# Kernel tuning notes

Measured on AMD Instinct MI355X. Metric: run time of the kernel, lower is better.

The kernel has to match this reference:

```python
import jax, jax.numpy as jnp
import numpy as np

N, E, IN_DIM, H, D = 40000, 640000, 128, 8, 16


def setup_inputs() -> dict:
    key = jax.random.key(0)
    k_h, k_s, k_d, k_q, k_k, k_v = jax.random.split(key, 6)
    scale = float(np.sqrt(2.0 / (IN_DIM + H * D)))  # xavier-ish
    return {
        "h": jax.random.normal(k_h, (N, IN_DIM), dtype=jnp.float32),
        "src": jax.random.randint(k_s, (E,), 0, N, dtype=jnp.int32),
        "dst": jax.random.randint(k_d, (E,), 0, N, dtype=jnp.int32),
        "WQ": jax.random.normal(k_q, (IN_DIM, H * D), dtype=jnp.float32) * scale,
        "WK": jax.random.normal(k_k, (IN_DIM, H * D), dtype=jnp.float32) * scale,
        "WV": jax.random.normal(k_v, (IN_DIM, H * D), dtype=jnp.float32) * scale,
    }


def reference(h, src, dst, WQ, WK, WV):
    n = h.shape[0]
    Q = (h @ WQ).reshape(n, H, D)  # [N,H,D]
    K = (h @ WK).reshape(n, H, D)
    V = (h @ WV).reshape(n, H, D)
    inv_sqrt_d = 1.0 / jnp.sqrt(jnp.asarray(D, dtype=h.dtype))
    # per-edge elementwise score (DGL u_mul_v keeps the H x D vector)
    score = K[src] * Q[dst] * inv_sqrt_d  # [E,H,D]
    wV = jax.ops.segment_sum(V[src] * score, dst, num_segments=n)  # [N,H,D]
    z = jax.ops.segment_sum(score, dst, num_segments=n)            # [N,H,D]
    return wV / (z + 1e-6)
```

## Files before the change

### kernel.cpp

```cpp
#include <hip/hip_runtime.h>


#define FMA4(acc, s, b) do { \
    (acc).x = fmaf((s), (b).x, (acc).x); \
    (acc).y = fmaf((s), (b).y, (acc).y); \
    (acc).z = fmaf((s), (b).z, (acc).z); \
    (acc).w = fmaf((s), (b).w, (acc).w); } while (0)

__global__ __launch_bounds__(256) void gemm_qkv(
    const float* __restrict__ h,
    const float* __restrict__ WQ,
    const float* __restrict__ WK,
    const float* __restrict__ WV,
    float* __restrict__ Qf,
    float* __restrict__ Kf,
    float* __restrict__ Vf,
    int N)
{
    __shared__ float4 Wl[128 * 32];
    __shared__ float4 Hl[32 * 32];
    const int t = threadIdx.x;
    const int which = blockIdx.y;
    const float* Wsel = (which == 0) ? WQ : ((which == 1) ? WK : WV);
    float* Osel = (which == 0) ? Qf : ((which == 1) ? Kf : Vf);
    const float4* W4 = (const float4*)Wsel;
#pragma unroll
    for (int i = 0; i < 16; ++i) Wl[t + i * 256] = W4[t + i * 256];

    const int c4 = t & 31;
    const int r4 = t >> 5;

    for (int sub = 0; sub < 4; ++sub) {
        const int r0 = (blockIdx.x * 4 + sub) * 32;
        if (r0 >= N) break;
        __syncthreads();
        const float4* H4 = (const float4*)(h + (size_t)r0 * 128);
#pragma unroll
        for (int i = 0; i < 4; ++i) Hl[t + i * 256] = H4[t + i * 256];
        __syncthreads();

        float4 acc0 = make_float4(0.f, 0.f, 0.f, 0.f);
        float4 acc1 = acc0, acc2 = acc0, acc3 = acc0;
#pragma unroll 8
        for (int k4 = 0; k4 < 32; ++k4) {
            float4 b0 = Wl[(k4 * 4 + 0) * 32 + c4];
            float4 b1 = Wl[(k4 * 4 + 1) * 32 + c4];
            float4 b2 = Wl[(k4 * 4 + 2) * 32 + c4];
            float4 b3 = Wl[(k4 * 4 + 3) * 32 + c4];
            float4 a0 = Hl[(r4 * 4 + 0) * 32 + k4];
            float4 a1 = Hl[(r4 * 4 + 1) * 32 + k4];
            float4 a2 = Hl[(r4 * 4 + 2) * 32 + k4];
            float4 a3 = Hl[(r4 * 4 + 3) * 32 + k4];
            FMA4(acc0, a0.x, b0); FMA4(acc0, a0.y, b1); FMA4(acc0, a0.z, b2); FMA4(acc0, a0.w, b3);
            FMA4(acc1, a1.x, b0); FMA4(acc1, a1.y, b1); FMA4(acc1, a1.z, b2); FMA4(acc1, a1.w, b3);
            FMA4(acc2, a2.x, b0); FMA4(acc2, a2.y, b1); FMA4(acc2, a2.z, b2); FMA4(acc2, a2.w, b3);
            FMA4(acc3, a3.x, b0); FMA4(acc3, a3.y, b1); FMA4(acc3, a3.z, b2); FMA4(acc3, a3.w, b3);
        }
        const int row = r0 + r4 * 4;
        float4* O = (float4*)Osel;
        O[(size_t)(row + 0) * 32 + c4] = acc0;
        O[(size_t)(row + 1) * 32 + c4] = acc1;
        O[(size_t)(row + 2) * 32 + c4] = acc2;
        O[(size_t)(row + 3) * 32 + c4] = acc3;
    }
}

__global__ __launch_bounds__(256) void count_deg(
    const int* __restrict__ dst, int* __restrict__ deg, int E)
{
    const int e = blockIdx.x * 256 + threadIdx.x;
    if (e < E) atomicAdd(&deg[dst[e]], 1);
}

__global__ __launch_bounds__(256) void chunk_reduce(
    const int* __restrict__ deg, int* __restrict__ csum, int N)
{
    const int t = threadIdx.x;
    const int i = blockIdx.x * 256 + t;
    int x = (i < N) ? deg[i] : 0;
#pragma unroll
    for (int off = 32; off; off >>= 1) x += __shfl_down(x, off, 64);
    __shared__ int ws[4];
    if ((t & 63) == 0) ws[t >> 6] = x;
    __syncthreads();
    if (t == 0) csum[blockIdx.x] = ws[0] + ws[1] + ws[2] + ws[3];
}

__global__ __launch_bounds__(256) void scan_chunks(
    const int* __restrict__ csum, int* __restrict__ coff, int nChunks)
{
    __shared__ int s[256];
    __shared__ int carry;
    const int t = threadIdx.x;
    if (t == 0) carry = 0;
    __syncthreads();
    for (int base = 0; base < nChunks; base += 256) {
        const int i = base + t;
        int x = (i < nChunks) ? csum[i] : 0;
        s[t] = x;
        __syncthreads();
        for (int off = 1; off < 256; off <<= 1) {
            int v = (t >= off) ? s[t - off] : 0;
            __syncthreads();
            s[t] += v;
            __syncthreads();
        }
        if (i < nChunks) coff[i] = carry + s[t] - x;
        __syncthreads();
        if (t == 0) carry += s[255];
        __syncthreads();
    }
}

__global__ __launch_bounds__(256) void chunk_scan(
    const int* __restrict__ deg, const int* __restrict__ coff,
    int* __restrict__ rowptr, int N)
{
    __shared__ int s[256];
    const int t = threadIdx.x;
    const int i = blockIdx.x * 256 + t;
    int x = (i < N) ? deg[i] : 0;
    s[t] = x;
    __syncthreads();
    for (int off = 1; off < 256; off <<= 1) {
        int v = (t >= off) ? s[t - off] : 0;
        __syncthreads();
        s[t] += v;
        __syncthreads();
    }
    if (i < N) rowptr[i + 1] = coff[blockIdx.x] + s[t];
    if (i == 0) rowptr[0] = 0;
}

__global__ __launch_bounds__(256) void scatter_eids(
    const int* __restrict__ dst, const int* __restrict__ rowptr,
    int* __restrict__ cur, int* __restrict__ eids, int E)
{
    const int e = blockIdx.x * 256 + threadIdx.x;
    if (e >= E) return;
    const int d = dst[e];
    const int pos = rowptr[d] + atomicAdd(&cur[d], 1);
    eids[pos] = e;
}

__global__ __launch_bounds__(256) void sort_lists(
    const int* __restrict__ rowptr, int* __restrict__ eids, int N)
{
    const int n = blockIdx.x * 256 + threadIdx.x;
    if (n >= N) return;
    const int lo = rowptr[n], hi = rowptr[n + 1];
    for (int i = lo + 1; i < hi; ++i) {
        const int key = eids[i];
        int j = i - 1;
        while (j >= lo && eids[j] > key) { eids[j + 1] = eids[j]; --j; }
        eids[j + 1] = key;
    }
}

__global__ __launch_bounds__(128) void attn_out(
    const int* __restrict__ src, const int* __restrict__ rowptr,
    const int* __restrict__ eids,
    const float* __restrict__ Kf, const float* __restrict__ Qf,
    const float* __restrict__ Vf,
    float* __restrict__ out, int N)
{
#pragma clang fp contract(off)
    const int d = blockIdx.x;
    const int c = threadIdx.x;
    const float q = Qf[(size_t)d * 128 + c];
    const int lo = rowptr[d], hi = rowptr[d + 1];
    float z = 0.f, wv = 0.f;
    for (int i = lo; i < hi; ++i) {
        const int e = eids[i];
        const int s = src[e];
        const float k = Kf[(size_t)s * 128 + c];
        const float v = Vf[(size_t)s * 128 + c];
        const float sc = (k * q) * 0.25f;
        z = z + sc;
        const float p = v * sc;
        wv = wv + p;
    }
    out[(size_t)d * 128 + c] = wv / (z + 1e-6f);
}

extern "C" void kernel_launch(void* const* d_in, const int* in_sizes, int n_in,
                              void* d_out, int out_size, void* d_ws, size_t ws_size,
                              hipStream_t stream)
{
    const float* h  = (const float*)d_in[0];
    const int* src  = (const int*)d_in[1];
    const int* dst  = (const int*)d_in[2];
    const float* WQ = (const float*)d_in[3];
    const float* WK = (const float*)d_in[4];
    const float* WV = (const float*)d_in[5];
    const int N = in_sizes[0] / 128;
    const int E = in_sizes[1];
    const size_t NC = (size_t)N * 128;
    const int nChunks = (N + 255) / 256;

    float* Kf = (float*)d_ws;
    float* Qf = Kf + NC;
    float* Vf = Qf + NC;
    int* deg    = (int*)(Vf + NC);
    int* cur    = deg + N;
    int* rowptr = cur + N;
    int* eids   = rowptr + (N + 1);
    int* csum   = eids + E;
    int* coff   = csum + nChunks;
    float* outp = (float*)d_out;

    hipMemsetAsync(deg, 0, (size_t)2 * N * sizeof(int), stream);

    dim3 ggrid((N + 127) / 128, 3);
    gemm_qkv<<<ggrid, 256, 0, stream>>>(h, WQ, WK, WV, Qf, Kf, Vf, N);

    const int eb = (E + 255) / 256;
    count_deg<<<eb, 256, 0, stream>>>(dst, deg, E);
    chunk_reduce<<<nChunks, 256, 0, stream>>>(deg, csum, N);
    scan_chunks<<<1, 256, 0, stream>>>(csum, coff, nChunks);
    chunk_scan<<<nChunks, 256, 0, stream>>>(deg, coff, rowptr, N);
    scatter_eids<<<eb, 256, 0, stream>>>(dst, rowptr, cur, eids, E);
    sort_lists<<<(N + 255) / 256, 256, 0, stream>>>(rowptr, eids, N);

    attn_out<<<N, 128, 0, stream>>>(src, rowptr, eids, Kf, Qf, Vf, outp, N);
}
```

Baseline: 350.0 us.

## Interleave K/V rows, pre-gather source ids, and unroll edge loop with float2

The GEMM now writes K and V interleaved per node, so one gathered row holds both and the attention kernel touches a single contiguous 1KB region per source. The scatter step stores (edge, src) pairs and the sort step emits a sorted src array, which removes the dependent eids->src indirection from the hot loop. The attention kernel uses 64 threads with float2 loads and unrolls four edges so more gathers are in flight. Per-edge summation order is unchanged, so results stay bitwise identical. The cost is extra workspace and a wider sort payload.

```diff
diff --git a/kernel.cpp b/kernel.cpp
--- a/kernel.cpp
+++ b/kernel.cpp
@@ -13,8 +13,7 @@
     const float* __restrict__ WK,
     const float* __restrict__ WV,
     float* __restrict__ Qf,
-    float* __restrict__ Kf,
-    float* __restrict__ Vf,
+    float* __restrict__ KV,
     int N)
 {
     __shared__ float4 Wl[128 * 32];
@@ -22,13 +21,15 @@
     const int t = threadIdx.x;
     const int which = blockIdx.y;
     const float* Wsel = (which == 0) ? WQ : ((which == 1) ? WK : WV);
-    float* Osel = (which == 0) ? Qf : ((which == 1) ? Kf : Vf);
     const float4* W4 = (const float4*)Wsel;
 #pragma unroll
     for (int i = 0; i < 16; ++i) Wl[t + i * 256] = W4[t + i * 256];
 
     const int c4 = t & 31;
     const int r4 = t >> 5;
+    float4* Obase = (which == 0) ? (float4*)Qf : (float4*)KV;
+    const int ostride = (which == 0) ? 32 : 64;
+    const int ooff = (which == 2) ? 32 : 0;
 
     for (int sub = 0; sub < 4; ++sub) {
         const int r0 = (blockIdx.x * 4 + sub) * 32;
@@ -57,11 +58,10 @@
             FMA4(acc3, a3.x, b0); FMA4(acc3, a3.y, b1); FMA4(acc3, a3.z, b2); FMA4(acc3, a3.w, b3);
         }
         const int row = r0 + r4 * 4;
-        float4* O = (float4*)Osel;
-        O[(size_t)(row + 0) * 32 + c4] = acc0;
-        O[(size_t)(row + 1) * 32 + c4] = acc1;
-        O[(size_t)(row + 2) * 32 + c4] = acc2;
-        O[(size_t)(row + 3) * 32 + c4] = acc3;
+        Obase[(size_t)(row + 0) * ostride + ooff + c4] = acc0;
+        Obase[(size_t)(row + 1) * ostride + ooff + c4] = acc1;
+        Obase[(size_t)(row + 2) * ostride + ooff + c4] = acc2;
+        Obase[(size_t)(row + 3) * ostride + ooff + c4] = acc3;
     }
 }
 
@@ -132,55 +132,73 @@
     if (i == 0) rowptr[0] = 0;
 }
 
-__global__ __launch_bounds__(256) void scatter_eids(
-    const int* __restrict__ dst, const int* __restrict__ rowptr,
-    int* __restrict__ cur, int* __restrict__ eids, int E)
+__global__ __launch_bounds__(256) void scatter_pairs(
+    const int* __restrict__ dst, const int* __restrict__ src,
+    const int* __restrict__ rowptr, int* __restrict__ cur,
+    int2* __restrict__ pairs, int E)
 {
     const int e = blockIdx.x * 256 + threadIdx.x;
     if (e >= E) return;
     const int d = dst[e];
     const int pos = rowptr[d] + atomicAdd(&cur[d], 1);
-    eids[pos] = e;
-}
-
-__global__ __launch_bounds__(256) void sort_lists(
-    const int* __restrict__ rowptr, int* __restrict__ eids, int N)
+    pairs[pos] = make_int2(e, src[e]);
+}
+
+__global__ __launch_bounds__(256) void sort_emit_srcs(
+    const int* __restrict__ rowptr, int2* __restrict__ pairs,
+    int* __restrict__ srcs, int N)
 {
     const int n = blockIdx.x * 256 + threadIdx.x;
     if (n >= N) return;
     const int lo = rowptr[n], hi = rowptr[n + 1];
     for (int i = lo + 1; i < hi; ++i) {
-        const int key = eids[i];
+        const int2 key = pairs[i];
         int j = i - 1;
-        while (j >= lo && eids[j] > key) { eids[j + 1] = eids[j]; --j; }
-        eids[j + 1] = key;
-    }
-}
-
-__global__ __launch_bounds__(128) void attn_out(
-    const int* __restrict__ src, const int* __restrict__ rowptr,
-    const int* __restrict__ eids,
-    const float* __restrict__ Kf, const float* __restrict__ Qf,
-    const float* __restrict__ Vf,
+        while (j >= lo && pairs[j].x > key.x) { pairs[j + 1] = pairs[j]; --j; }
+        pairs[j + 1] = key;
+    }
+    for (int i = lo; i < hi; ++i) srcs[i] = pairs[i].y;
+}
+
+__global__ __launch_bounds__(64) void attn_out(
+    const int* __restrict__ srcs, const int* __restrict__ rowptr,
+    const float* __restrict__ KV, const float* __restrict__ Qf,
     float* __restrict__ out, int N)
 {
 #pragma clang fp contract(off)
     const int d = blockIdx.x;
     const int c = threadIdx.x;
-    const float q = Qf[(size_t)d * 128 + c];
+    const float2 q = ((const float2*)Qf)[(size_t)d * 64 + c];
     const int lo = rowptr[d], hi = rowptr[d + 1];
-    float z = 0.f, wv = 0.f;
-    for (int i = lo; i < hi; ++i) {
-        const int e = eids[i];
-        const int s = src[e];
-        const float k = Kf[(size_t)s * 128 + c];
-        const float v = Vf[(size_t)s * 128 + c];
-        const float sc = (k * q) * 0.25f;
-        z = z + sc;
-        const float p = v * sc;
-        wv = wv + p;
-    }
-    out[(size_t)d * 128 + c] = wv / (z + 1e-6f);
+    const float2* KV2 = (const float2*)KV;
+    float2 z = make_float2(0.f, 0.f), wv = z;
+
+#define EDGE_UPD(k, v) do { \
+        float sc0 = ((k).x * q.x) * 0.25f; z.x = z.x + sc0; wv.x = wv.x + (v).x * sc0; \
+        float sc1 = ((k).y * q.y) * 0.25f; z.y = z.y + sc1; wv.y = wv.y + (v).y * sc1; \
+    } while (0)
+
+    int i = lo;
+    for (; i + 4 <= hi; i += 4) {
+        const int s0 = srcs[i + 0], s1 = srcs[i + 1];
+        const int s2 = srcs[i + 2], s3 = srcs[i + 3];
+        const float2 k0 = KV2[(size_t)s0 * 128 + c], v0 = KV2[(size_t)s0 * 128 + 64 + c];
+        const float2 k1 = KV2[(size_t)s1 * 128 + c], v1 = KV2[(size_t)s1 * 128 + 64 + c];
+        const float2 k2 = KV2[(size_t)s2 * 128 + c], v2 = KV2[(size_t)s2 * 128 + 64 + c];
+        const float2 k3 = KV2[(size_t)s3 * 128 + c], v3 = KV2[(size_t)s3 * 128 + 64 + c];
+        EDGE_UPD(k0, v0); EDGE_UPD(k1, v1); EDGE_UPD(k2, v2); EDGE_UPD(k3, v3);
+    }
+    for (; i < hi; ++i) {
+        const int s = srcs[i];
+        const float2 k = KV2[(size_t)s * 128 + c], v = KV2[(size_t)s * 128 + 64 + c];
+        EDGE_UPD(k, v);
+    }
+#undef EDGE_UPD
+
+    float2 o;
+    o.x = wv.x / (z.x + 1e-6f);
+    o.y = wv.y / (z.y + 1e-6f);
+    ((float2*)out)[(size_t)d * 64 + c] = o;
 }
 
 extern "C" void kernel_launch(void* const* d_in, const int* in_sizes, int n_in,
@@ -198,29 +216,29 @@
     const size_t NC = (size_t)N * 128;
     const int nChunks = (N + 255) / 256;
 
-    float* Kf = (float*)d_ws;
-    float* Qf = Kf + NC;
-    float* Vf = Qf + NC;
-    int* deg    = (int*)(Vf + NC);
+    float* KV = (float*)d_ws;
+    float* Qf = KV + (size_t)N * 256;
+    int* deg    = (int*)(Qf + NC);
     int* cur    = deg + N;
     int* rowptr = cur + N;
-    int* eids   = rowptr + (N + 1);
-    int* csum   = eids + E;
+    int* csum   = rowptr + (N + 1);
     int* coff   = csum + nChunks;
+    int* srcs   = coff + nChunks;
+    int2* pairs = (int2*)(srcs + E);
     float* outp = (float*)d_out;
 
     hipMemsetAsync(deg, 0, (size_t)2 * N * sizeof(int), stream);
 
     dim3 ggrid((N + 127) / 128, 3);
-    gemm_qkv<<<ggrid, 256, 0, stream>>>(h, WQ, WK, WV, Qf, Kf, Vf, N);
+    gemm_qkv<<<ggrid, 256, 0, stream>>>(h, WQ, WK, WV, Qf, KV, N);
 
     const int eb = (E + 255) / 256;
     count_deg<<<eb, 256, 0, stream>>>(dst, deg, E);
     chunk_reduce<<<nChunks, 256, 0, stream>>>(deg, csum, N);
     scan_chunks<<<1, 256, 0, stream>>>(csum, coff, nChunks);
     chunk_scan<<<nChunks, 256, 0, stream>>>(deg, coff, rowptr, N);
-    scatter_eids<<<eb, 256, 0, stream>>>(dst, rowptr, cur, eids, E);
-    sort_lists<<<(N + 255) / 256, 256, 0, stream>>>(rowptr, eids, N);
-
-    attn_out<<<N, 128, 0, stream>>>(src, rowptr, eids, Kf, Qf, Vf, outp, N);
-}
+    scatter_pairs<<<eb, 256, 0, stream>>>(dst, src, rowptr, cur, pairs, E);
+    sort_emit_srcs<<<(N + 255) / 256, 256, 0, stream>>>(rowptr, pairs, srcs, N);
+
+    attn_out<<<N, 64, 0, stream>>>(srcs, rowptr, KV, Qf, outp, N);
+}
```

Result: faster. 336.2 us (-3.9%).
